# Kernel optimization log

Measured on AMD Instinct MI355X. Metric: run time of the kernel, lower is better.

## Reference

```python
import jax, jax.numpy as jnp
import numpy as np

EPS = 1e-5
GROUPS = 8


def setup_inputs() -> dict:
    key = jax.random.key(0)
    ks = jax.random.split(key, 4)
    b, c, h, w = 2, 64, 80, 80
    std = 0.02
    return {
        "x": jax.random.normal(ks[0], (b, c, h, w), dtype=jnp.float32),
        "g_w": jax.random.normal(ks[1], (c, c), dtype=jnp.float32) * std,
        "g_b": jnp.zeros((c,), dtype=jnp.float32),
        "w_w": jax.random.normal(ks[2], (c, c), dtype=jnp.float32) * std,
        "w_b": jnp.zeros((c,), dtype=jnp.float32),
        "gn_w": jax.random.normal(ks[3], (c,), dtype=jnp.float32) * std + 1.0,
        "gn_b": jnp.zeros((c,), dtype=jnp.float32),
    }


def reference(x, g_w, g_b, w_w, w_b, gn_w, gn_b):
    b, c, h, w = x.shape
    n = h * w
    xf = x.reshape(b, c, n)                                   # (b,c,N)
    # g: 1x1 conv -> (b,N,Ci) after permute
    g_x = jnp.einsum('ic,bcn->bni', g_w, xf) + g_b            # (b,N,Ci)
    # theta == phi == flattened x (inter_channels == in_channels)
    aff = jnp.einsum('bcn,bcm->bnm', xf, xf)                  # (b,N,N)
    score = jax.nn.sigmoid(aff)                               # (b,N,N)
    emb = jnp.einsum('bnm,bmi->bni', score, g_x)              # (b,N,Ci)
    emb = emb.transpose(0, 2, 1).reshape(b, c, h, w)          # (b,Ci,h,w)
    # W: 1x1 conv + GroupNorm(8, C)
    y = jnp.einsum('oc,bchw->bohw', w_w, emb) + w_b[None, :, None, None]
    yg = y.reshape(b, GROUPS, c // GROUPS, h, w)
    mean = yg.mean(axis=(2, 3, 4), keepdims=True)
    var = yg.var(axis=(2, 3, 4), keepdims=True)
    yn = ((yg - mean) / jnp.sqrt(var + EPS)).reshape(b, c, h, w)
    out = yn * gn_w[None, :, None, None] + gn_b[None, :, None, None]
    return (out, score)
```

## Files before the change

### kernel.cpp

```cpp
#include <hip/hip_runtime.h>
#include <cstddef>

namespace {
constexpr int B = 2;
constexpr int C = 64;
constexpr int N = 6400;
constexpr int NT = N / 64;
constexpr int MSPLIT = 5;
constexpr int MT_PER = NT / MSPLIT;
constexpr float EPS = 1e-5f;
constexpr int LS = 68;
constexpr int LSB = 72;
}

typedef __attribute__((ext_vector_type(8))) short short8;
typedef __attribute__((ext_vector_type(4))) float f32x4;
typedef __attribute__((ext_vector_type(4))) unsigned short us4v;
typedef __attribute__((ext_vector_type(8))) unsigned short us8v;

__device__ inline unsigned short f2bf(float f) {
  unsigned int u = __float_as_uint(f);
  u += 0x7fffu + ((u >> 16) & 1u);
  return (unsigned short)(u >> 16);
}
__device__ inline float bf2f(unsigned short u) {
  return __uint_as_float(((unsigned int)u) << 16);
}

__global__ __launch_bounds__(256) void xprep_kernel(
    const float* __restrict__ x, const float* __restrict__ g_w,
    const float* __restrict__ g_b, unsigned short* __restrict__ xT,
    unsigned short* __restrict__ gxT) {
  __shared__ float xs[64 * LS];
  __shared__ float gwt[64 * LS];
  const int b = blockIdx.x / NT;
  const int n0 = (blockIdx.x % NT) * 64;
  const int tid = threadIdx.x;
  const int col = tid & 63, row4 = tid >> 6;
  const float* xb = x + (size_t)b * C * N;
#pragma unroll
  for (int it = 0; it < 16; ++it) {
    int r = row4 + it * 4;
    xs[r * LS + col] = xb[(size_t)r * N + n0 + col];
    gwt[col * LS + r] = g_w[r * 64 + col];
  }
  __syncthreads();

  {
    const int ty = tid >> 4, tx = tid & 15;
    float acc[4][4];
#pragma unroll
    for (int a = 0; a < 4; ++a) {
      float gbv = g_b[ty * 4 + a];
      acc[a][0] = gbv; acc[a][1] = gbv; acc[a][2] = gbv; acc[a][3] = gbv;
    }
#pragma unroll 8
    for (int c = 0; c < 64; ++c) {
      const f32x4 a4 = *(const f32x4*)&gwt[c * LS + ty * 4];
      const f32x4 b4 = *(const f32x4*)&xs[c * LS + tx * 4];
#pragma unroll
      for (int a = 0; a < 4; ++a) {
        acc[a][0] += a4[a] * b4[0]; acc[a][1] += a4[a] * b4[1];
        acc[a][2] += a4[a] * b4[2]; acc[a][3] += a4[a] * b4[3];
      }
    }
    unsigned short* gxTb = gxT + (size_t)b * 64 * N;
#pragma unroll
    for (int a = 0; a < 4; ++a) {
      us4v v;
      v[0] = f2bf(acc[a][0]); v[1] = f2bf(acc[a][1]);
      v[2] = f2bf(acc[a][2]); v[3] = f2bf(acc[a][3]);
      *(us4v*)&gxTb[(size_t)(ty * 4 + a) * N + n0 + tx * 4] = v;
    }
  }

  {
    const int nloc = tid >> 2, cs = (tid & 3) * 16;
    us8v u0, u1;
#pragma unroll
    for (int j = 0; j < 8; ++j) u0[j] = f2bf(xs[(cs + j) * LS + nloc]);
#pragma unroll
    for (int j = 0; j < 8; ++j) u1[j] = f2bf(xs[(cs + 8 + j) * LS + nloc]);
    unsigned short* xTb = xT + (size_t)b * N * 64;
    *(us8v*)&xTb[(size_t)(n0 + nloc) * 64 + cs] = u0;
    *(us8v*)&xTb[(size_t)(n0 + nloc) * 64 + cs + 8] = u1;
  }
}

__global__ __launch_bounds__(256, 4) void relation_main(
    const unsigned short* __restrict__ xT, const unsigned short* __restrict__ gxT,
    float* __restrict__ score, float* __restrict__ emb_p) {
  __shared__ alignas(16) unsigned short xmT[64 * LSB];
  __shared__ alignas(16) unsigned short gxt[64 * LSB];
  __shared__ alignas(16) unsigned short sc[64 * LSB];

  const int tid = threadIdx.x;
  const int w = tid >> 6, lane = tid & 63;
  const int l15 = lane & 15, quad = lane >> 4;

  const int bIdx = blockIdx.x / (NT * MSPLIT);
  const int rest = blockIdx.x % (NT * MSPLIT);
  const int nt = rest / MSPLIT;
  const int ms = rest % MSPLIT;
  const int n0 = nt * 64;

  const unsigned short* xTb = xT + (size_t)bIdx * N * 64;
  const unsigned short* gxTb = gxT + (size_t)bIdx * 64 * N;
  float* scoreb = score + (size_t)bIdx * N * N;

  const short8 a0 = *(const short8*)&xTb[(size_t)(n0 + 16 * w + l15) * 64 + quad * 8];
  const short8 a1 = *(const short8*)&xTb[(size_t)(n0 + 16 * w + l15) * 64 + 32 + quad * 8];

  const int srow = tid >> 3, sco = (tid & 7) * 8;

  const int mbase = ms * MT_PER * 64;
  us8v xm0 = *(const us8v*)&xTb[(size_t)(mbase + srow) * 64 + sco];
  us8v xm1 = *(const us8v*)&xTb[(size_t)(mbase + srow + 32) * 64 + sco];
  us8v gx0 = *(const us8v*)&gxTb[(size_t)srow * N + mbase + sco];
  us8v gx1 = *(const us8v*)&gxTb[(size_t)(srow + 32) * N + mbase + sco];

  f32x4 e[4];
  const f32x4 zero = {0.f, 0.f, 0.f, 0.f};
#pragma unroll
  for (int is = 0; is < 4; ++is) e[is] = zero;

  for (int j = 0; j < MT_PER; ++j) {
    const int mj = (ms * MT_PER + j) * 64;
    __syncthreads();
    *(us8v*)&xmT[srow * LSB + sco] = xm0;
    *(us8v*)&xmT[(srow + 32) * LSB + sco] = xm1;
    *(us8v*)&gxt[srow * LSB + sco] = gx0;
    *(us8v*)&gxt[(srow + 32) * LSB + sco] = gx1;
    __syncthreads();
    if (j + 1 < MT_PER) {
      const int m1 = mj + 64;
      xm0 = *(const us8v*)&xTb[(size_t)(m1 + srow) * 64 + sco];
      xm1 = *(const us8v*)&xTb[(size_t)(m1 + srow + 32) * 64 + sco];
      gx0 = *(const us8v*)&gxTb[(size_t)srow * N + m1 + sco];
      gx1 = *(const us8v*)&gxTb[(size_t)(srow + 32) * N + m1 + sco];
    }

    f32x4 s[4];
#pragma unroll
    for (int msub = 0; msub < 4; ++msub) {
      short8 b0 = *(const short8*)&xmT[(16 * msub + l15) * LSB + quad * 8];
      short8 b1 = *(const short8*)&xmT[(16 * msub + l15) * LSB + 32 + quad * 8];
      f32x4 d = __builtin_amdgcn_mfma_f32_16x16x32_bf16(a0, b0, zero, 0, 0, 0);
      s[msub] = __builtin_amdgcn_mfma_f32_16x16x32_bf16(a1, b1, d, 0, 0, 0);
    }

    float* sp = scoreb + (size_t)(n0 + 16 * w + quad * 4) * N + mj + l15;
#pragma unroll
    for (int msub = 0; msub < 4; ++msub) {
#pragma unroll
      for (int r = 0; r < 4; ++r) {
        float t = __builtin_amdgcn_exp2f(-1.442695041f * s[msub][r]);
        float sig = __builtin_amdgcn_rcpf(1.f + t);
        sc[(16 * w + quad * 4 + r) * LSB + 16 * msub + l15] = f2bf(sig);
        sp[(size_t)r * N + 16 * msub] = sig;
      }
    }

    short8 p0 = *(const short8*)&sc[(16 * w + l15) * LSB + quad * 8];
    short8 p1 = *(const short8*)&sc[(16 * w + l15) * LSB + 32 + quad * 8];
#pragma unroll
    for (int is = 0; is < 4; ++is) {
      short8 g0 = *(const short8*)&gxt[(16 * is + l15) * LSB + quad * 8];
      short8 g1 = *(const short8*)&gxt[(16 * is + l15) * LSB + 32 + quad * 8];
      e[is] = __builtin_amdgcn_mfma_f32_16x16x32_bf16(p0, g0, e[is], 0, 0, 0);
      e[is] = __builtin_amdgcn_mfma_f32_16x16x32_bf16(p1, g1, e[is], 0, 0, 0);
    }
  }

  float* ep = emb_p + ((size_t)ms * B + bIdx) * (size_t)N * 64;
#pragma unroll
  for (int is = 0; is < 4; ++is) {
#pragma unroll
    for (int r = 0; r < 4; ++r) {
      ep[(size_t)(n0 + 16 * w + quad * 4 + r) * 64 + 16 * is + l15] = e[is][r];
    }
  }
}

__global__ __launch_bounds__(256) void y_kernel(
    const float* __restrict__ emb_p, const float* __restrict__ w_w,
    const float* __restrict__ w_b, float* __restrict__ y) {
  __shared__ float embT[64 * LS];
  __shared__ float wt[64 * LS];
  const int b = blockIdx.x / NT;
  const int n0 = (blockIdx.x % NT) * 64;
  const int tid = threadIdx.x;
  const int col = tid & 63, row4 = tid >> 6;
  const int ty = tid >> 4, tx = tid & 15;
#pragma unroll
  for (int it = 0; it < 16; ++it) {
    int r = row4 + it * 4;
    wt[col * LS + r] = w_w[r * 64 + col];
    float v = 0.f;
#pragma unroll
    for (int msv = 0; msv < MSPLIT; ++msv)
      v += emb_p[((size_t)msv * B + b) * N * C + (size_t)(n0 + r) * C + col];
    embT[col * LS + r] = v;
  }
  __syncthreads();
  float acc[4][4];
#pragma unroll
  for (int a = 0; a < 4; ++a) {
    float wbv = w_b[ty * 4 + a];
    acc[a][0] = wbv; acc[a][1] = wbv; acc[a][2] = wbv; acc[a][3] = wbv;
  }
#pragma unroll 8
  for (int i = 0; i < 64; ++i) {
    const f32x4 w4 = *(const f32x4*)&wt[i * LS + ty * 4];
    const f32x4 e4 = *(const f32x4*)&embT[i * LS + tx * 4];
#pragma unroll
    for (int a = 0; a < 4; ++a) {
      acc[a][0] += w4[a] * e4[0]; acc[a][1] += w4[a] * e4[1];
      acc[a][2] += w4[a] * e4[2]; acc[a][3] += w4[a] * e4[3];
    }
  }
  float* yb = y + (size_t)b * C * N;
#pragma unroll
  for (int a = 0; a < 4; ++a) {
    f32x4 v = {acc[a][0], acc[a][1], acc[a][2], acc[a][3]};
    *(f32x4*)&yb[(size_t)(ty * 4 + a) * N + n0 + tx * 4] = v;
  }
}

__global__ __launch_bounds__(256) void stats_kernel(const float* __restrict__ y,
                                                    float* __restrict__ stats) {
  const int bg = blockIdx.x;
  const f32x4* p = (const f32x4*)(y + (size_t)bg * 8 * N);
  float s = 0.f, q = 0.f;
  for (int i = threadIdx.x; i < 8 * N / 4; i += 256) {
    f32x4 v = p[i];
    s += v[0] + v[1] + v[2] + v[3];
    q += v[0] * v[0] + v[1] * v[1] + v[2] * v[2] + v[3] * v[3];
  }
#pragma unroll
  for (int off = 32; off > 0; off >>= 1) {
    s += __shfl_down(s, off, 64);
    q += __shfl_down(q, off, 64);
  }
  __shared__ float ls[4], lq[4];
  const int lane = threadIdx.x & 63, wv = threadIdx.x >> 6;
  if (lane == 0) { ls[wv] = s; lq[wv] = q; }
  __syncthreads();
  if (threadIdx.x == 0) {
    float S = ls[0] + ls[1] + ls[2] + ls[3];
    float Q = lq[0] + lq[1] + lq[2] + lq[3];
    const float inv = 1.f / (float)(8 * N);
    float mean = S * inv;
    float var = Q * inv - mean * mean;
    stats[bg * 2 + 0] = mean;
    stats[bg * 2 + 1] = rsqrtf(var + EPS);
  }
}

__global__ __launch_bounds__(256) void norm_kernel(
    const float* __restrict__ y, const float* __restrict__ stats,
    const float* __restrict__ gn_w, const float* __restrict__ gn_b,
    float* __restrict__ out) {
  const int idx = blockIdx.x * 256 + threadIdx.x;
  const int e0 = idx * 4;
  const int b = e0 / (C * N);
  const int c = (e0 / N) & 63;
  const int g = c >> 3;
  const float mean = stats[(b * 8 + g) * 2 + 0];
  const float rstd = stats[(b * 8 + g) * 2 + 1];
  const float w = gn_w[c] * rstd;
  const float bb = gn_b[c] - mean * w;
  f32x4 v = *(const f32x4*)&y[e0];
  v[0] = v[0] * w + bb; v[1] = v[1] * w + bb;
  v[2] = v[2] * w + bb; v[3] = v[3] * w + bb;
  *(f32x4*)&out[e0] = v;
}

extern "C" void kernel_launch(void* const* d_in, const int* in_sizes, int n_in,
                              void* d_out, int out_size, void* d_ws, size_t ws_size,
                              hipStream_t stream) {
  const float* x    = (const float*)d_in[0];
  const float* g_w  = (const float*)d_in[1];
  const float* g_b  = (const float*)d_in[2];
  const float* w_w  = (const float*)d_in[3];
  const float* w_b  = (const float*)d_in[4];
  const float* gn_w = (const float*)d_in[5];
  const float* gn_b = (const float*)d_in[6];
  (void)in_sizes; (void)n_in; (void)out_size; (void)ws_size;

  float* out   = (float*)d_out;
  float* score = out + (size_t)B * C * N;

  float* ws    = (float*)d_ws;
  float* emb_p = ws;
  float* y     = emb_p + (size_t)MSPLIT * B * N * C;
  float* stats = y + (size_t)B * C * N;
  unsigned short* xT  = (unsigned short*)(stats + 32);
  unsigned short* gxT = xT + (size_t)B * N * 64;

  hipLaunchKernelGGL(xprep_kernel, dim3(B * NT), dim3(256), 0, stream,
                     x, g_w, g_b, xT, gxT);
  hipLaunchKernelGGL(relation_main, dim3(B * NT * MSPLIT), dim3(256), 0, stream,
                     xT, gxT, score, emb_p);
  hipLaunchKernelGGL(y_kernel, dim3(B * NT), dim3(256), 0, stream, emb_p, w_w, w_b, y);
  hipLaunchKernelGGL(stats_kernel, dim3(B * 8), dim3(256), 0, stream, y, stats);
  hipLaunchKernelGGL(norm_kernel, dim3((B * C * N) / 1024), dim3(256), 0, stream,
                     y, stats, gn_w, gn_b, out);
}
```

Baseline: 398.0 us.

## Restructure relation kernel to 128-row tiles, sync-free global operand loads, vector stores

The relation kernel now gives each block 128 query rows, 32 per wave, and holds that wave's x fragments in registers. The key (m) fragments of x and g(x) are read straight from global memory instead of being staged through shared memory with two barriers per iteration. The affinity MFMA is transposed so each lane writes four contiguous score floats and emb outputs as 16-byte vector stores. MSPLIT rises to 10 to keep enough blocks in flight, which doubles the emb partial workspace and the reduction work in y_kernel. Occupancy is lowered to 3 blocks per SIMD-unit hint.

```diff
diff --git a/kernel.cpp b/kernel.cpp
--- a/kernel.cpp
+++ b/kernel.cpp
@@ -6,7 +6,8 @@
 constexpr int C = 64;
 constexpr int N = 6400;
 constexpr int NT = N / 64;
-constexpr int MSPLIT = 5;
+constexpr int NT2 = N / 128;
+constexpr int MSPLIT = 10;
 constexpr int MT_PER = NT / MSPLIT;
 constexpr float EPS = 1e-5f;
 constexpr int LS = 68;
@@ -22,9 +23,6 @@
   unsigned int u = __float_as_uint(f);
   u += 0x7fffu + ((u >> 16) & 1u);
   return (unsigned short)(u >> 16);
-}
-__device__ inline float bf2f(unsigned short u) {
-  return __uint_as_float(((unsigned int)u) << 16);
 }
 
 __global__ __launch_bounds__(256) void xprep_kernel(
@@ -87,99 +85,87 @@
   }
 }
 
-__global__ __launch_bounds__(256, 4) void relation_main(
+__global__ __launch_bounds__(256, 3) void relation_main(
     const unsigned short* __restrict__ xT, const unsigned short* __restrict__ gxT,
     float* __restrict__ score, float* __restrict__ emb_p) {
-  __shared__ alignas(16) unsigned short xmT[64 * LSB];
-  __shared__ alignas(16) unsigned short gxt[64 * LSB];
-  __shared__ alignas(16) unsigned short sc[64 * LSB];
+  __shared__ alignas(16) unsigned short sc[128 * LSB];
 
   const int tid = threadIdx.x;
   const int w = tid >> 6, lane = tid & 63;
   const int l15 = lane & 15, quad = lane >> 4;
 
-  const int bIdx = blockIdx.x / (NT * MSPLIT);
-  const int rest = blockIdx.x % (NT * MSPLIT);
+  const int bIdx = blockIdx.x / (NT2 * MSPLIT);
+  const int rest = blockIdx.x % (NT2 * MSPLIT);
   const int nt = rest / MSPLIT;
   const int ms = rest % MSPLIT;
-  const int n0 = nt * 64;
+  const int nw = nt * 128 + 32 * w;
 
   const unsigned short* xTb = xT + (size_t)bIdx * N * 64;
   const unsigned short* gxTb = gxT + (size_t)bIdx * 64 * N;
   float* scoreb = score + (size_t)bIdx * N * N;
 
-  const short8 a0 = *(const short8*)&xTb[(size_t)(n0 + 16 * w + l15) * 64 + quad * 8];
-  const short8 a1 = *(const short8*)&xTb[(size_t)(n0 + 16 * w + l15) * 64 + 32 + quad * 8];
-
-  const int srow = tid >> 3, sco = (tid & 7) * 8;
-
-  const int mbase = ms * MT_PER * 64;
-  us8v xm0 = *(const us8v*)&xTb[(size_t)(mbase + srow) * 64 + sco];
-  us8v xm1 = *(const us8v*)&xTb[(size_t)(mbase + srow + 32) * 64 + sco];
-  us8v gx0 = *(const us8v*)&gxTb[(size_t)srow * N + mbase + sco];
-  us8v gx1 = *(const us8v*)&gxTb[(size_t)(srow + 32) * N + mbase + sco];
-
-  f32x4 e[4];
+  short8 bn[2][2];
+#pragma unroll
+  for (int ns = 0; ns < 2; ++ns)
+#pragma unroll
+    for (int ks = 0; ks < 2; ++ks)
+      bn[ns][ks] =
+          *(const short8*)&xTb[(size_t)(nw + 16 * ns + l15) * 64 + ks * 32 + quad * 8];
+
+  f32x4 e[4][2];
   const f32x4 zero = {0.f, 0.f, 0.f, 0.f};
 #pragma unroll
-  for (int is = 0; is < 4; ++is) e[is] = zero;
+  for (int is = 0; is < 4; ++is) { e[is][0] = zero; e[is][1] = zero; }
 
   for (int j = 0; j < MT_PER; ++j) {
     const int mj = (ms * MT_PER + j) * 64;
-    __syncthreads();
-    *(us8v*)&xmT[srow * LSB + sco] = xm0;
-    *(us8v*)&xmT[(srow + 32) * LSB + sco] = xm1;
-    *(us8v*)&gxt[srow * LSB + sco] = gx0;
-    *(us8v*)&gxt[(srow + 32) * LSB + sco] = gx1;
-    __syncthreads();
-    if (j + 1 < MT_PER) {
-      const int m1 = mj + 64;
-      xm0 = *(const us8v*)&xTb[(size_t)(m1 + srow) * 64 + sco];
-      xm1 = *(const us8v*)&xTb[(size_t)(m1 + srow + 32) * 64 + sco];
-      gx0 = *(const us8v*)&gxTb[(size_t)srow * N + m1 + sco];
-      gx1 = *(const us8v*)&gxTb[(size_t)(srow + 32) * N + m1 + sco];
-    }
-
-    f32x4 s[4];
+
 #pragma unroll
     for (int msub = 0; msub < 4; ++msub) {
-      short8 b0 = *(const short8*)&xmT[(16 * msub + l15) * LSB + quad * 8];
-      short8 b1 = *(const short8*)&xmT[(16 * msub + l15) * LSB + 32 + quad * 8];
-      f32x4 d = __builtin_amdgcn_mfma_f32_16x16x32_bf16(a0, b0, zero, 0, 0, 0);
-      s[msub] = __builtin_amdgcn_mfma_f32_16x16x32_bf16(a1, b1, d, 0, 0, 0);
-    }
-
-    float* sp = scoreb + (size_t)(n0 + 16 * w + quad * 4) * N + mj + l15;
-#pragma unroll
-    for (int msub = 0; msub < 4; ++msub) {
-#pragma unroll
-      for (int r = 0; r < 4; ++r) {
-        float t = __builtin_amdgcn_exp2f(-1.442695041f * s[msub][r]);
-        float sig = __builtin_amdgcn_rcpf(1.f + t);
-        sc[(16 * w + quad * 4 + r) * LSB + 16 * msub + l15] = f2bf(sig);
-        sp[(size_t)r * N + 16 * msub] = sig;
+      const unsigned short* amp = &xTb[(size_t)(mj + 16 * msub + l15) * 64 + quad * 8];
+      short8 am0 = *(const short8*)&amp[0];
+      short8 am1 = *(const short8*)&amp[32];
+#pragma unroll
+      for (int ns = 0; ns < 2; ++ns) {
+        f32x4 d = __builtin_amdgcn_mfma_f32_16x16x32_bf16(am0, bn[ns][0], zero, 0, 0, 0);
+        d = __builtin_amdgcn_mfma_f32_16x16x32_bf16(am1, bn[ns][1], d, 0, 0, 0);
+        f32x4 sg; us4v sb;
+#pragma unroll
+        for (int r = 0; r < 4; ++r) {
+          float t = __builtin_amdgcn_exp2f(-1.442695041f * d[r]);
+          sg[r] = __builtin_amdgcn_rcpf(1.f + t);
+          sb[r] = f2bf(sg[r]);
+        }
+        *(f32x4*)&scoreb[(size_t)(nw + 16 * ns + l15) * N + mj + 16 * msub + quad * 4] = sg;
+        *(us4v*)&sc[(32 * w + 16 * ns + l15) * LSB + 16 * msub + quad * 4] = sb;
       }
     }
 
-    short8 p0 = *(const short8*)&sc[(16 * w + l15) * LSB + quad * 8];
-    short8 p1 = *(const short8*)&sc[(16 * w + l15) * LSB + 32 + quad * 8];
+    short8 p[2][2];
+#pragma unroll
+    for (int ns = 0; ns < 2; ++ns) {
+      p[ns][0] = *(const short8*)&sc[(32 * w + 16 * ns + l15) * LSB + quad * 8];
+      p[ns][1] = *(const short8*)&sc[(32 * w + 16 * ns + l15) * LSB + 32 + quad * 8];
+    }
 #pragma unroll
     for (int is = 0; is < 4; ++is) {
-      short8 g0 = *(const short8*)&gxt[(16 * is + l15) * LSB + quad * 8];
-      short8 g1 = *(const short8*)&gxt[(16 * is + l15) * LSB + 32 + quad * 8];
-      e[is] = __builtin_amdgcn_mfma_f32_16x16x32_bf16(p0, g0, e[is], 0, 0, 0);
-      e[is] = __builtin_amdgcn_mfma_f32_16x16x32_bf16(p1, g1, e[is], 0, 0, 0);
+      const unsigned short* gp = &gxTb[(size_t)(16 * is + l15) * N + mj + quad * 8];
+      short8 g0 = *(const short8*)&gp[0];
+      short8 g1 = *(const short8*)&gp[32];
+#pragma unroll
+      for (int ns = 0; ns < 2; ++ns) {
+        e[is][ns] = __builtin_amdgcn_mfma_f32_16x16x32_bf16(g0, p[ns][0], e[is][ns], 0, 0, 0);
+        e[is][ns] = __builtin_amdgcn_mfma_f32_16x16x32_bf16(g1, p[ns][1], e[is][ns], 0, 0, 0);
+      }
     }
   }
 
   float* ep = emb_p + ((size_t)ms * B + bIdx) * (size_t)N * 64;
 #pragma unroll
-  for (int is = 0; is < 4; ++is) {
-#pragma unroll
-    for (int r = 0; r < 4; ++r) {
-      ep[(size_t)(n0 + 16 * w + quad * 4 + r) * 64 + 16 * is + l15] = e[is][r];
-    }
-  }
+  for (int is = 0; is < 4; ++is)
+#pragma unroll
+    for (int ns = 0; ns < 2; ++ns)
+      *(f32x4*)&ep[(size_t)(nw + 16 * ns + l15) * 64 + 16 * is + quad * 4] = e[is][ns];
 }
 
 __global__ __launch_bounds__(256) void y_kernel(
@@ -300,7 +286,7 @@
 
   hipLaunchKernelGGL(xprep_kernel, dim3(B * NT), dim3(256), 0, stream,
                      x, g_w, g_b, xT, gxT);
-  hipLaunchKernelGGL(relation_main, dim3(B * NT * MSPLIT), dim3(256), 0, stream,
+  hipLaunchKernelGGL(relation_main, dim3(B * NT2 * MSPLIT), dim3(256), 0, stream,
                      xT, gxT, score, emb_p);
   hipLaunchKernelGGL(y_kernel, dim3(B * NT), dim3(256), 0, stream, emb_p, w_w, w_b, y);
   hipLaunchKernelGGL(stats_kernel, dim3(B * 8), dim3(256), 0, stream, y, stats);
```

New measurement: 458.7 us. 1.15x slower.

## Swap MFMA operand order so each lane writes contiguous score and emb vectors

Applied to the files above, without the earlier changes.

The MFMA operands are swapped (m-tile as A, n-rows as B) so each lane's accumulator holds four consecutive columns of one row. This lets the score output and the emb partials be written as 16-byte float4 stores, and the bf16 sigmoid tile be written to LDS as one 8-byte store. It also fuses the sigmoid and store loop into the MFMA loop, and replaces __syncthreads with explicit lgkmcnt waits, raw barriers and a sched_barrier. The cost being targeted is the scattered scalar stores of the large score matrix; the new layout changes the global write pattern per wavefront, and the sched_barrier limits compiler reordering.

```diff
diff --git a/kernel.cpp b/kernel.cpp
--- a/kernel.cpp
+++ b/kernel.cpp
@@ -22,9 +22,6 @@
   unsigned int u = __float_as_uint(f);
   u += 0x7fffu + ((u >> 16) & 1u);
   return (unsigned short)(u >> 16);
-}
-__device__ inline float bf2f(unsigned short u) {
-  return __uint_as_float(((unsigned int)u) << 16);
 }
 
 __global__ __launch_bounds__(256) void xprep_kernel(
@@ -103,13 +100,14 @@
   const int nt = rest / MSPLIT;
   const int ms = rest % MSPLIT;
   const int n0 = nt * 64;
+  const int nw = n0 + 16 * w;
 
   const unsigned short* xTb = xT + (size_t)bIdx * N * 64;
   const unsigned short* gxTb = gxT + (size_t)bIdx * 64 * N;
   float* scoreb = score + (size_t)bIdx * N * N;
 
-  const short8 a0 = *(const short8*)&xTb[(size_t)(n0 + 16 * w + l15) * 64 + quad * 8];
-  const short8 a1 = *(const short8*)&xTb[(size_t)(n0 + 16 * w + l15) * 64 + 32 + quad * 8];
+  short8 bn0 = *(const short8*)&xTb[(size_t)(nw + l15) * 64 + quad * 8];
+  short8 bn1 = *(const short8*)&xTb[(size_t)(nw + l15) * 64 + 32 + quad * 8];
 
   const int srow = tid >> 3, sco = (tid & 7) * 8;
 
@@ -126,12 +124,17 @@
 
   for (int j = 0; j < MT_PER; ++j) {
     const int mj = (ms * MT_PER + j) * 64;
-    __syncthreads();
+
+    asm volatile("s_waitcnt lgkmcnt(0)" ::: "memory");
+    __builtin_amdgcn_s_barrier();
     *(us8v*)&xmT[srow * LSB + sco] = xm0;
     *(us8v*)&xmT[(srow + 32) * LSB + sco] = xm1;
     *(us8v*)&gxt[srow * LSB + sco] = gx0;
     *(us8v*)&gxt[(srow + 32) * LSB + sco] = gx1;
-    __syncthreads();
+    asm volatile("s_waitcnt lgkmcnt(0)" ::: "memory");
+    __builtin_amdgcn_s_barrier();
+    __builtin_amdgcn_sched_barrier(0);
+
     if (j + 1 < MT_PER) {
       const int m1 = mj + 64;
       xm0 = *(const us8v*)&xTb[(size_t)(m1 + srow) * 64 + sco];
@@ -140,25 +143,21 @@
       gx1 = *(const us8v*)&gxTb[(size_t)(srow + 32) * N + m1 + sco];
     }
 
-    f32x4 s[4];
 #pragma unroll
     for (int msub = 0; msub < 4; ++msub) {
-      short8 b0 = *(const short8*)&xmT[(16 * msub + l15) * LSB + quad * 8];
-      short8 b1 = *(const short8*)&xmT[(16 * msub + l15) * LSB + 32 + quad * 8];
-      f32x4 d = __builtin_amdgcn_mfma_f32_16x16x32_bf16(a0, b0, zero, 0, 0, 0);
-      s[msub] = __builtin_amdgcn_mfma_f32_16x16x32_bf16(a1, b1, d, 0, 0, 0);
-    }
-
-    float* sp = scoreb + (size_t)(n0 + 16 * w + quad * 4) * N + mj + l15;
-#pragma unroll
-    for (int msub = 0; msub < 4; ++msub) {
+      short8 am0 = *(const short8*)&xmT[(16 * msub + l15) * LSB + quad * 8];
+      short8 am1 = *(const short8*)&xmT[(16 * msub + l15) * LSB + 32 + quad * 8];
+      f32x4 d = __builtin_amdgcn_mfma_f32_16x16x32_bf16(am0, bn0, zero, 0, 0, 0);
+      d = __builtin_amdgcn_mfma_f32_16x16x32_bf16(am1, bn1, d, 0, 0, 0);
+      f32x4 sg; us4v sb;
 #pragma unroll
       for (int r = 0; r < 4; ++r) {
-        float t = __builtin_amdgcn_exp2f(-1.442695041f * s[msub][r]);
-        float sig = __builtin_amdgcn_rcpf(1.f + t);
-        sc[(16 * w + quad * 4 + r) * LSB + 16 * msub + l15] = f2bf(sig);
-        sp[(size_t)r * N + 16 * msub] = sig;
+        float t = __builtin_amdgcn_exp2f(-1.442695041f * d[r]);
+        sg[r] = __builtin_amdgcn_rcpf(1.f + t);
+        sb[r] = f2bf(sg[r]);
       }
+      *(f32x4*)&scoreb[(size_t)(nw + l15) * N + mj + 16 * msub + quad * 4] = sg;
+      *(us4v*)&sc[(16 * w + l15) * LSB + 16 * msub + quad * 4] = sb;
     }
 
     short8 p0 = *(const short8*)&sc[(16 * w + l15) * LSB + quad * 8];
@@ -167,19 +166,15 @@
     for (int is = 0; is < 4; ++is) {
       short8 g0 = *(const short8*)&gxt[(16 * is + l15) * LSB + quad * 8];
       short8 g1 = *(const short8*)&gxt[(16 * is + l15) * LSB + 32 + quad * 8];
-      e[is] = __builtin_amdgcn_mfma_f32_16x16x32_bf16(p0, g0, e[is], 0, 0, 0);
-      e[is] = __builtin_amdgcn_mfma_f32_16x16x32_bf16(p1, g1, e[is], 0, 0, 0);
+      e[is] = __builtin_amdgcn_mfma_f32_16x16x32_bf16(g0, p0, e[is], 0, 0, 0);
+      e[is] = __builtin_amdgcn_mfma_f32_16x16x32_bf16(g1, p1, e[is], 0, 0, 0);
     }
   }
 
   float* ep = emb_p + ((size_t)ms * B + bIdx) * (size_t)N * 64;
 #pragma unroll
-  for (int is = 0; is < 4; ++is) {
-#pragma unroll
-    for (int r = 0; r < 4; ++r) {
-      ep[(size_t)(n0 + 16 * w + quad * 4 + r) * 64 + 16 * is + l15] = e[is][r];
-    }
-  }
+  for (int is = 0; is < 4; ++is)
+    *(f32x4*)&ep[(size_t)(nw + l15) * 64 + 16 * is + quad * 4] = e[is];
 }
 
 __global__ __launch_bounds__(256) void y_kernel(
```

After: 394.8 us. Within noise of the previous version (-0.8%).
